# Kernel optimization log

Measured on AMD Instinct MI355X. Metric: run time of the kernel, lower is better.

The kernel has to match this reference:

```python
import jax, jax.numpy as jnp
import numpy as np

H, T, D = 16, 2048, 1024
DH = D // H  # 64


def setup_inputs() -> dict:
    key = jax.random.key(0)
    ks = jax.random.split(key, 6)
    state = jax.random.normal(ks[0], (H, DH, DH), jnp.float32) * 0.02  # per-head recurrent state
    x = jax.random.normal(ks[1], (T, D), jnp.float32)
    done = jax.random.uniform(ks[2], (T,)) < (4.0 / T)  # sparse episode-reset flags (bool)
    w_qkv = jax.random.normal(ks[3], (D, 3 * D), jnp.float32) / np.sqrt(D)
    b_qkv = jnp.zeros((3 * D,), jnp.float32)
    w_out = jax.random.normal(ks[4], (D, D), jnp.float32) / np.sqrt(D)
    b_out = jnp.zeros((D,), jnp.float32)
    return {"state": state, "x": x, "done": done, "w_qkv": w_qkv,
            "b_qkv": b_qkv, "w_out": w_out, "b_out": b_out}


def _mha_forward(state, x, done, w_qkv, b_qkv, w_out, b_out):
    # qkv projection; einops 'T (QKV H Dh) -> QKV H T Dh'
    qkv = (x @ w_qkv + b_qkv).reshape(T, 3, H, DH).transpose(1, 2, 0, 3)
    q, k, v = qkv[0], qkv[1], qkv[2]  # each (H, T, Dh)

    cum = jnp.cumsum(done.astype(jnp.int32))  # inclusive cumsum, as in done.cumsum()
    before_first = cum == 0            # tokens before first reset (attend to carried state)
    after_last = cum == cum[-1]        # tokens after last reset (feed new state)
    done_any = cum[-1] > 0

    # make_attn_mask(done): causal AND no reset index i with s < i <= t.
    # The scanned mask equals: causal & (cum[t] == cum[s]) (same-segment).
    t_idx = jnp.arange(T)
    mask = (t_idx[:, None] >= t_idx[None, :]) & (cum[:, None] == cum[None, :])  # (T, T)

    attn = jnp.where(mask[None], jnp.einsum('htd,hsd->hts', q, k), 0.0)  # mask * (q @ k.T)
    q_bef = q * before_first[None, :, None]
    out = jnp.einsum('hts,hsd->htd', attn, v) + jnp.einsum('htd,hde->hte', q_bef, state)

    k_aft = k * after_last[None, :, None]
    v_aft = v * after_last[None, :, None]
    s_new = jnp.einsum('htd,hte->hde', k_aft, v_aft)  # k_aft.T @ v_aft per head
    new_state = jnp.where(done_any, s_new, state + s_new)

    # 'H T Dh -> T (H Dh)' then output projection
    x_out = out.transpose(1, 0, 2).reshape(T, D) @ w_out + b_out
    return new_state, x_out


def reference(state, x, done, w_qkv, b_qkv, w_out, b_out):
    return _mha_forward(state, x, done, w_qkv, b_qkv, w_out, b_out)
```

## Files before the change

### kernel.cpp

```cpp
#include <hip/hip_runtime.h>

#define TT 2048
#define DD 1024
#define HH 16
#define DH 64
#define QKV_N 3072
#define QKW 2048

typedef __attribute__((ext_vector_type(8))) short bf16x8;
typedef __attribute__((ext_vector_type(4))) short short4v;
typedef __attribute__((ext_vector_type(4))) float f32x4;

__device__ inline short f2bf(float f) {
    union { float f; unsigned u; } v; v.f = f;
    unsigned r = v.u + 0x7fff + ((v.u >> 16) & 1);
    return (short)(r >> 16);
}

__device__ inline f32x4 mfma16(bf16x8 a, bf16x8 b, f32x4 c) {
    return __builtin_amdgcn_mfma_f32_16x16x32_bf16(a, b, c, 0, 0, 0);
}

__device__ __forceinline__ void gload16(const void* g, void* l) {
    __builtin_amdgcn_global_load_lds(
        (const __attribute__((address_space(1))) unsigned int*)g,
        (__attribute__((address_space(3))) unsigned int*)l, 16, 0, 0);
}

__device__ void transpose_tile(const float* __restrict__ in, short* __restrict__ out,
                               int R, int C, int r0, int c0, float (*tile)[65]) {
    int tid = threadIdx.x;
#pragma unroll
    for (int p = 0; p < 4; ++p) {
        int ch = tid + p * 256;
        int r = ch >> 4, c4 = (ch & 15) * 4;
        float4 v = *(const float4*)&in[(size_t)(r0 + r) * C + c0 + c4];
        tile[r][c4] = v.x; tile[r][c4 + 1] = v.y; tile[r][c4 + 2] = v.z; tile[r][c4 + 3] = v.w;
    }
    __syncthreads();
#pragma unroll
    for (int p = 0; p < 2; ++p) {
        int ch = tid + p * 256;
        int c = ch >> 3, r8 = (ch & 7) * 8;
        short tmp[8];
#pragma unroll
        for (int i = 0; i < 8; ++i) tmp[i] = f2bf(tile[r8 + i][c]);
        *(float4*)&out[(size_t)(c0 + c) * R + r0 + r8] = *(float4*)tmp;
    }
}

__global__ __launch_bounds__(256) void prep_kernel(const float* __restrict__ x,
                                                   const float* __restrict__ w_qkv,
                                                   const float* __restrict__ w_out,
                                                   const float* __restrict__ state,
                                                   const int* __restrict__ done,
                                                   short* __restrict__ x_bf,
                                                   short* __restrict__ wqT,
                                                   short* __restrict__ woT,
                                                   short* __restrict__ stT,
                                                   float* __restrict__ stout,
                                                   int* __restrict__ seg,
                                                   int* __restrict__ totalp,
                                                   int* __restrict__ aux) {
    __shared__ float tile[64][65];
    __shared__ int scanbuf[2048 + 512 + 1];
    int b = blockIdx.x;
    int tid = threadIdx.x;
    if (b < 1024) {
        int i = (b * 256 + tid) * 8;
        float4 a = *(const float4*)&x[i];
        float4 c = *(const float4*)&x[i + 4];
        short tmp[8] = {f2bf(a.x), f2bf(a.y), f2bf(a.z), f2bf(a.w),
                        f2bf(c.x), f2bf(c.y), f2bf(c.z), f2bf(c.w)};
        *(float4*)&x_bf[i] = *(float4*)tmp;
    } else if (b < 1792) {
        int bb = b - 1024;
        transpose_tile(w_qkv, wqT, DD, QKV_N, (bb & 15) * 64, (bb >> 4) * 64, tile);
    } else if (b < 2048) {
        int bb = b - 1792;
        transpose_tile(w_out, woT, DD, DD, (bb & 15) * 64, (bb >> 4) * 64, tile);
    } else if (b < 2064) {
        int h = b - 2048;
        transpose_tile(state + (size_t)h * 4096, stT + (size_t)h * 4096, DH, DH, 0, 0, tile);
    } else if (b < 2128) {
        __shared__ int anyf;
        if (tid == 0) anyf = 0;
        __syncthreads();
        int acc = 0;
#pragma unroll
        for (int i = 0; i < 8; ++i) acc |= done[tid * 8 + i];
        if (acc) anyf = 1;
        __syncthreads();
        int f = ((b - 2064) * 256 + tid) * 4;
        float4 v = anyf ? make_float4(0.f, 0.f, 0.f, 0.f) : *(const float4*)&state[f];
        *(float4*)&stout[f] = v;
    } else {
        int* segl = scanbuf;
        int* part = scanbuf + 2048;
        int* excl = scanbuf + 2304;
        int base = tid * 8;
        int local[8];
        int run = 0;
#pragma unroll
        for (int i = 0; i < 8; ++i) { run += (done[base + i] != 0) ? 1 : 0; local[i] = run; }
        part[tid] = run;
        __syncthreads();
        if (tid < 64) {
            int p4[4];
#pragma unroll
            for (int i = 0; i < 4; ++i) p4[i] = part[tid * 4 + i];
            int s = p4[0] + p4[1] + p4[2] + p4[3];
            int v = s;
#pragma unroll
            for (int off = 1; off < 64; off <<= 1) {
                int u = __shfl_up(v, off);
                if (tid >= off) v += u;
            }
            int ex = v - s;
#pragma unroll
            for (int i = 0; i < 4; ++i) { excl[tid * 4 + i] = ex; ex += p4[i]; }
            if (tid == 63) { totalp[0] = v; scanbuf[2560] = v; }
        }
        __syncthreads();
        int off = excl[tid];
#pragma unroll
        for (int i = 0; i < 8; ++i) {
            int sv = off + local[i];
            seg[base + i] = sv;
            segl[base + i] = sv;
        }
        __syncthreads();
        if (tid < 33) {
            int target = (tid < 32) ? segl[tid * 64] : scanbuf[2560];
            int lo = 0, hi = 2047;
            while (lo < hi) { int mid = (lo + hi) >> 1; if (segl[mid] >= target) hi = mid; else lo = mid + 1; }
            aux[tid] = lo >> 6;
        }
    }
}

__global__ __launch_bounds__(256) void gemm_qkv(const short* __restrict__ A,
                                                const short* __restrict__ BT,
                                                const float* __restrict__ bias,
                                                short* __restrict__ qk,
                                                short* __restrict__ vt) {
    __shared__ __align__(16) short As[128 * 32];
    __shared__ __align__(16) short Bs[128 * 32];
    const int K = DD;
    int tid = threadIdx.x;
    int wave = tid >> 6, lane = tid & 63;
    int quad = lane >> 4, l15 = lane & 15;
    int m0 = blockIdx.x * 128, n0 = blockIdx.y * 128;
    int wr = (wave >> 1) * 64, wc = (wave & 1) * 64;

    int srow = wave * 16 + (lane >> 2);
    int scol = (lane & 3) * 8;
    const short* Ag = A + (size_t)(m0 + srow) * K + scol;
    const short* Bg = BT + (size_t)(n0 + srow) * K + scol;
    short* As0 = &As[(wave * 16) * 32];
    short* As1 = &As[(64 + wave * 16) * 32];
    short* Bs0 = &Bs[(wave * 16) * 32];
    short* Bs1 = &Bs[(64 + wave * 16) * 32];

    f32x4 acc[4][4] = {};
    for (int k0 = 0; k0 < K; k0 += 32) {
        __syncthreads();
        gload16(Ag + k0, As0);
        gload16(Ag + (size_t)64 * K + k0, As1);
        gload16(Bg + k0, Bs0);
        gload16(Bg + (size_t)64 * K + k0, Bs1);
        __syncthreads();
        bf16x8 af[4], bfr[4];
#pragma unroll
        for (int i = 0; i < 4; ++i) {
            af[i]  = *(const bf16x8*)&As[(wr + i * 16 + l15) * 32 + quad * 8];
            bfr[i] = *(const bf16x8*)&Bs[(wc + i * 16 + l15) * 32 + quad * 8];
        }
#pragma unroll
        for (int i = 0; i < 4; ++i)
#pragma unroll
            for (int j = 0; j < 4; ++j)
                acc[i][j] = mfma16(af[i], bfr[j], acc[i][j]);
    }

    if (n0 < 2048) {
#pragma unroll
        for (int i = 0; i < 4; ++i)
#pragma unroll
            for (int j = 0; j < 4; ++j)
#pragma unroll
                for (int r = 0; r < 4; ++r) {
                    int row = m0 + wr + i * 16 + quad * 4 + r;
                    int col = n0 + wc + j * 16 + l15;
                    qk[(size_t)row * QKW + col] = f2bf(acc[i][j][r] + bias[col]);
                }
    } else {
#pragma unroll
        for (int j = 0; j < 4; ++j) {
            int col = n0 + wc + j * 16 + l15;
            float bv = bias[col];
            int eg = col - 2048;
            int hh = eg >> 6, e = eg & 63;
#pragma unroll
            for (int i = 0; i < 4; ++i) {
                int tb = m0 + wr + i * 16 + quad * 4;
                short4v pk;
#pragma unroll
                for (int r = 0; r < 4; ++r) pk[r] = f2bf(acc[i][j][r] + bv);
                *(short4v*)&vt[(size_t)hh * (DH * TT) + (size_t)e * TT + tb] = pk;
            }
        }
    }
}

__global__ __launch_bounds__(256) void attn_mfma(const short* __restrict__ qk,
                                                 const short* __restrict__ vt,
                                                 const short* __restrict__ stT,
                                                 const int* __restrict__ seg,
                                                 const int* __restrict__ totalp,
                                                 const int* __restrict__ aux,
                                                 short* __restrict__ outb,
                                                 float* __restrict__ nsout) {
    __shared__ __align__(16) short Qh[2][128 * 32];
    __shared__ __align__(16) short Kh[2][2][64 * 32];
    __shared__ __align__(16) short Vh[2][2][64 * 32];
    __shared__ __align__(16) short Ss[128 * 72];

    int h = blockIdx.x, tb = blockIdx.y;
    int t0 = tb * 128;
    int tid = threadIdx.x, wave = tid >> 6, lane = tid & 63;
    int quad = lane >> 4, l15 = lane & 15;
    int myt = wave * 32;
    const short* vbase = vt + (size_t)h * (DH * TT);

    if (blockIdx.z == 1) {
        int total = totalp[0];
        int myd = wave * 16;
        short* KhS0 = Kh[0][0];
        short* KhS1 = Kh[0][1];
#pragma unroll
        for (int cc = 0; cc < 2; ++cc) {
            int ct = tb * 2 + cc;
            if (ct < aux[32]) continue;
            int t0c = ct * 64;
            bool keep = (seg[t0c + lane] == total);
            const short* src = qk + (size_t)(t0c + lane) * QKW + 1024 + h * DH + myd;
            union { float4 f; short s[8]; } u0, u1;
            u0.f = keep ? *(const float4*)src : make_float4(0.f, 0.f, 0.f, 0.f);
            u1.f = keep ? *(const float4*)(src + 8) : make_float4(0.f, 0.f, 0.f, 0.f);
            short* dst = (lane < 32) ? &KhS0[lane] : &KhS1[lane - 32];
#pragma unroll
            for (int i = 0; i < 8; ++i) {
                dst[(myd + i) * 32] = u0.s[i];
                dst[(myd + 8 + i) * 32] = u1.s[i];
            }
            bf16x8 a0 = *(const bf16x8*)&KhS0[(myd + l15) * 32 + quad * 8];
            bf16x8 a1 = *(const bf16x8*)&KhS1[(myd + l15) * 32 + quad * 8];
            f32x4 acc2[4] = {};
#pragma unroll
            for (int j = 0; j < 4; ++j) {
                const short* vrow = vbase + (size_t)(j * 16 + l15) * TT + t0c + quad * 8;
                bf16x8 b0 = *(const bf16x8*)vrow;
                bf16x8 b1 = *(const bf16x8*)(vrow + 32);
                acc2[j] = mfma16(a0, b0, acc2[j]);
                acc2[j] = mfma16(a1, b1, acc2[j]);
            }
            float* oh = nsout + (size_t)h * 4096;
#pragma unroll
            for (int j = 0; j < 4; ++j)
#pragma unroll
                for (int r = 0; r < 4; ++r)
                    atomicAdd(&oh[(myd + quad * 4 + r) * DH + j * 16 + l15], acc2[j][r]);
        }
        return;
    }

    int st0 = aux[2 * tb];
    int st_hi = 2 * tb + 1;

    int srow = wave * 16 + (lane >> 2);
    int chunk = (lane & 3);
    const short* kg = qk + 1024 + h * DH;

    {
        int sr = (lane >> 2);
#pragma unroll
        for (int h2 = 0; h2 < 2; ++h2)
#pragma unroll
            for (int q = 0; q < 2; ++q)
                gload16(qk + (size_t)(t0 + myt + q * 16 + sr) * QKW + h * DH + h2 * 32 + chunk * 8,
                        &Qh[h2][(myt + q * 16) * 32]);
        int s0 = st0 * 64;
        gload16(kg + (size_t)(s0 + srow) * QKW + chunk * 8,      &Kh[0][0][(wave * 16) * 32]);
        gload16(kg + (size_t)(s0 + srow) * QKW + 32 + chunk * 8, &Kh[0][1][(wave * 16) * 32]);
        gload16(vbase + (size_t)srow * TT + s0 + chunk * 8,      &Vh[0][0][(wave * 16) * 32]);
        gload16(vbase + (size_t)srow * TT + s0 + 32 + chunk * 8, &Vh[0][1][(wave * 16) * 32]);
    }
    __syncthreads();

    bf16x8 af[2][2];
#pragma unroll
    for (int i = 0; i < 2; ++i)
#pragma unroll
        for (int h2 = 0; h2 < 2; ++h2)
            af[i][h2] = *(const bf16x8*)&Qh[h2][(myt + i * 16 + l15) * 32 + quad * 8];

    int seg_lane[2], t_val[2];
#pragma unroll
    for (int i = 0; i < 2; ++i) {
        t_val[i] = t0 + myt + i * 16 + l15;
        seg_lane[i] = seg[t_val[i]];
    }

    f32x4 acc2[4][2] = {};
    if (seg[t0] == 0) {
        const short* sb = stT + (size_t)h * 4096;
#pragma unroll
        for (int j = 0; j < 4; ++j)
#pragma unroll
            for (int h2 = 0; h2 < 2; ++h2) {
                bf16x8 a = *(const bf16x8*)(sb + (j * 16 + l15) * 64 + h2 * 32 + quad * 8);
#pragma unroll
                for (int i = 0; i < 2; ++i)
                    acc2[j][i] = mfma16(a, af[i][h2], acc2[j][i]);
            }
#pragma unroll
        for (int i = 0; i < 2; ++i)
            if (seg_lane[i] != 0)
#pragma unroll
                for (int j = 0; j < 4; ++j)
#pragma unroll
                    for (int r = 0; r < 4; ++r) acc2[j][i][r] = 0.f;
    }

    int p = 0;
    for (int st = st0; st <= st_hi; ++st, p ^= 1) {
        if (st != st0) __syncthreads();
        if (st + 1 <= st_hi) {
            int s1 = (st + 1) * 64;
            gload16(kg + (size_t)(s1 + srow) * QKW + chunk * 8,      &Kh[p ^ 1][0][(wave * 16) * 32]);
            gload16(kg + (size_t)(s1 + srow) * QKW + 32 + chunk * 8, &Kh[p ^ 1][1][(wave * 16) * 32]);
            gload16(vbase + (size_t)srow * TT + s1 + chunk * 8,      &Vh[p ^ 1][0][(wave * 16) * 32]);
            gload16(vbase + (size_t)srow * TT + s1 + 32 + chunk * 8, &Vh[p ^ 1][1][(wave * 16) * 32]);
        }
        int s0 = st * 64;

        f32x4 sacc[2][4] = {};
#pragma unroll
        for (int j = 0; j < 4; ++j)
#pragma unroll
            for (int h2 = 0; h2 < 2; ++h2) {
                bf16x8 kb = *(const bf16x8*)&Kh[p][h2][(j * 16 + l15) * 32 + quad * 8];
#pragma unroll
                for (int i = 0; i < 2; ++i)
                    sacc[i][j] = mfma16(kb, af[i][h2], sacc[i][j]);
            }
        int4 seg4[4];
#pragma unroll
        for (int j = 0; j < 4; ++j)
            seg4[j] = *(const int4*)&seg[s0 + j * 16 + quad * 4];
#pragma unroll
        for (int i = 0; i < 2; ++i)
#pragma unroll
            for (int j = 0; j < 4; ++j) {
                short4v pk;
#pragma unroll
                for (int r = 0; r < 4; ++r) {
                    int s_val = s0 + j * 16 + quad * 4 + r;
                    int sv = (r == 0) ? seg4[j].x : (r == 1) ? seg4[j].y : (r == 2) ? seg4[j].z : seg4[j].w;
                    bool ok = (sv == seg_lane[i]) && (s_val <= t_val[i]);
                    pk[r] = ok ? f2bf(sacc[i][j][r]) : (short)0;
                }
                *(short4v*)&Ss[(myt + i * 16 + l15) * 72 + j * 16 + quad * 4] = pk;
            }
        bf16x8 sf[2][2];
#pragma unroll
        for (int i = 0; i < 2; ++i)
#pragma unroll
            for (int h2 = 0; h2 < 2; ++h2)
                sf[i][h2] = *(const bf16x8*)&Ss[(myt + i * 16 + l15) * 72 + h2 * 32 + quad * 8];
#pragma unroll
        for (int j = 0; j < 4; ++j)
#pragma unroll
            for (int h2 = 0; h2 < 2; ++h2) {
                bf16x8 vb = *(const bf16x8*)&Vh[p][h2][(j * 16 + l15) * 32 + quad * 8];
#pragma unroll
                for (int i = 0; i < 2; ++i)
                    acc2[j][i] = mfma16(vb, sf[i][h2], acc2[j][i]);
            }
    }

#pragma unroll
    for (int i = 0; i < 2; ++i)
#pragma unroll
        for (int j = 0; j < 4; ++j) {
            short4v pk;
#pragma unroll
            for (int r = 0; r < 4; ++r) pk[r] = f2bf(acc2[j][i][r]);
            *(short4v*)&outb[(size_t)t_val[i] * DD + h * DH + j * 16 + quad * 4] = pk;
        }
}

__global__ __launch_bounds__(256) void gemm_out(const short* __restrict__ A,
                                                const short* __restrict__ BT,
                                                const float* __restrict__ bias,
                                                float* __restrict__ Cout,
                                                int M, int N, int K) {
    __shared__ __align__(16) short As[128 * 32];
    __shared__ __align__(16) short Bs[128 * 32];
    int tid = threadIdx.x;
    int wave = tid >> 6, lane = tid & 63;
    int quad = lane >> 4, l15 = lane & 15;
    int m0 = blockIdx.x * 128, n0 = blockIdx.y * 128;
    int wr = (wave >> 1) * 64, wc = (wave & 1) * 64;

    int srow = wave * 16 + (lane >> 2);
    int scol = (lane & 3) * 8;
    const short* Ag = A + (size_t)(m0 + srow) * K + scol;
    const short* Bg = BT + (size_t)(n0 + srow) * K + scol;
    short* As0 = &As[(wave * 16) * 32];
    short* As1 = &As[(64 + wave * 16) * 32];
    short* Bs0 = &Bs[(wave * 16) * 32];
    short* Bs1 = &Bs[(64 + wave * 16) * 32];

    f32x4 acc[4][4] = {};
    for (int k0 = 0; k0 < K; k0 += 32) {
        __syncthreads();
        gload16(Ag + k0, As0);
        gload16(Ag + (size_t)64 * K + k0, As1);
        gload16(Bg + k0, Bs0);
        gload16(Bg + (size_t)64 * K + k0, Bs1);
        __syncthreads();
        bf16x8 af[4], bfr[4];
#pragma unroll
        for (int i = 0; i < 4; ++i) {
            af[i]  = *(const bf16x8*)&As[(wr + i * 16 + l15) * 32 + quad * 8];
            bfr[i] = *(const bf16x8*)&Bs[(wc + i * 16 + l15) * 32 + quad * 8];
        }
#pragma unroll
        for (int i = 0; i < 4; ++i)
#pragma unroll
            for (int j = 0; j < 4; ++j)
                acc[i][j] = mfma16(af[i], bfr[j], acc[i][j]);
    }
#pragma unroll
    for (int i = 0; i < 4; ++i)
#pragma unroll
        for (int j = 0; j < 4; ++j)
#pragma unroll
            for (int r = 0; r < 4; ++r) {
                int row = m0 + wr + i * 16 + quad * 4 + r;
                int col = n0 + wc + j * 16 + l15;
                Cout[(size_t)row * N + col] = acc[i][j][r] + bias[col];
            }
}

extern "C" void kernel_launch(void* const* d_in, const int* in_sizes, int n_in,
                              void* d_out, int out_size, void* d_ws, size_t ws_size,
                              hipStream_t stream) {
    const float* state = (const float*)d_in[0];
    const float* x     = (const float*)d_in[1];
    const int*   done  = (const int*)d_in[2];
    const float* w_qkv = (const float*)d_in[3];
    const float* b_qkv = (const float*)d_in[4];
    const float* w_out = (const float*)d_in[5];
    const float* b_out = (const float*)d_in[6];

    char* ws = (char*)d_ws;
    int*   seg    = (int*)ws;
    int*   totalp = (int*)(ws + 8192);
    int*   aux    = (int*)(ws + 8256);
    short* wqT    = (short*)(ws + 8448);
    short* woT    = (short*)(ws + 6299904);
    short* stT    = (short*)(ws + 8397056);
    short* qk     = (short*)(ws + 8528128);
    short* vt     = (short*)(ws + 16916736);
    short* xbf_outb = (short*)(ws + 21111040);

    float* new_state_out = (float*)d_out;
    float* x_out         = (float*)d_out + HH * DH * DH;

    prep_kernel<<<2129, 256, 0, stream>>>(x, w_qkv, w_out, state, done,
                                          xbf_outb, wqT, woT, stT,
                                          new_state_out, seg, totalp, aux);

    gemm_qkv<<<dim3(TT / 128, QKV_N / 128), 256, 0, stream>>>(
        xbf_outb, wqT, b_qkv, qk, vt);

    attn_mfma<<<dim3(HH, TT / 128, 2), 256, 0, stream>>>(
        qk, vt, stT, seg, totalp, aux, xbf_outb, new_state_out);

    gemm_out<<<dim3(TT / 128, DD / 128), 256, 0, stream>>>(
        xbf_outb, woT, b_out, x_out, TT, DD, DD);
}
```

Baseline: 163.5 us.

## Split attention over key chunks with partial reduce, split-K output GEMM, wider QKV K-step

Attention now uses 64-token query tiles and splits the key range of each tile into chunks along grid z, writing fp32 partials that a new reduce kernel sums. The state-update path moves to its own z slice. The output GEMM becomes split-K by two with atomicAdd into an output that prep_kernel pre-fills with the bias. The QKV GEMM loads 64-wide K tiles per sync to halve barrier count. The aim is more parallelism and fewer idle CUs, at the cost of extra partial-buffer traffic, atomics and one more launch.

Result: faster. 159.4 us (-2.5%).

```diff
diff --git a/kernel.cpp b/kernel.cpp
--- a/kernel.cpp
+++ b/kernel.cpp
@@ -54,11 +54,13 @@
                                                    const float* __restrict__ w_out,
                                                    const float* __restrict__ state,
                                                    const int* __restrict__ done,
+                                                   const float* __restrict__ b_out,
                                                    short* __restrict__ x_bf,
                                                    short* __restrict__ wqT,
                                                    short* __restrict__ woT,
                                                    short* __restrict__ stT,
                                                    float* __restrict__ stout,
+                                                   float* __restrict__ x_out,
                                                    int* __restrict__ seg,
                                                    int* __restrict__ totalp,
                                                    int* __restrict__ aux) {
@@ -94,6 +96,10 @@
         int f = ((b - 2064) * 256 + tid) * 4;
         float4 v = anyf ? make_float4(0.f, 0.f, 0.f, 0.f) : *(const float4*)&state[f];
         *(float4*)&stout[f] = v;
+    } else if (b < 4176) {
+        int f = ((b - 2128) * 256 + tid) * 4;
+        int col = f & (DD - 1);
+        *(float4*)&x_out[f] = *(const float4*)&b_out[col];
     } else {
         int* segl = scanbuf;
         int* part = scanbuf + 2048;
@@ -144,13 +150,285 @@
                                                 const float* __restrict__ bias,
                                                 short* __restrict__ qk,
                                                 short* __restrict__ vt) {
-    __shared__ __align__(16) short As[128 * 32];
-    __shared__ __align__(16) short Bs[128 * 32];
+    __shared__ __align__(16) short As[2][128 * 32];
+    __shared__ __align__(16) short Bs[2][128 * 32];
     const int K = DD;
     int tid = threadIdx.x;
     int wave = tid >> 6, lane = tid & 63;
     int quad = lane >> 4, l15 = lane & 15;
     int m0 = blockIdx.x * 128, n0 = blockIdx.y * 128;
+    int wr = (wave >> 1) * 64, wc = (wave & 1) * 64;
+
+    int srow = wave * 32 + (lane >> 2);
+    int scol = (lane & 3) * 8;
+    const short* Ag = A + (size_t)(m0 + srow) * K + scol;
+    const short* Bg = BT + (size_t)(n0 + srow) * K + scol;
+
+    f32x4 acc[4][4] = {};
+    for (int k0 = 0; k0 < K; k0 += 64) {
+        __syncthreads();
+#pragma unroll
+        for (int g = 0; g < 2; ++g)
+#pragma unroll
+            for (int ks = 0; ks < 2; ++ks) {
+                gload16(Ag + (size_t)g * 16 * K + k0 + ks * 32, &As[ks][(wave * 32 + g * 16) * 32]);
+                gload16(Bg + (size_t)g * 16 * K + k0 + ks * 32, &Bs[ks][(wave * 32 + g * 16) * 32]);
+            }
+        __syncthreads();
+#pragma unroll
+        for (int ks = 0; ks < 2; ++ks) {
+            bf16x8 af[4], bfr[4];
+#pragma unroll
+            for (int i = 0; i < 4; ++i) {
+                af[i]  = *(const bf16x8*)&As[ks][(wr + i * 16 + l15) * 32 + quad * 8];
+                bfr[i] = *(const bf16x8*)&Bs[ks][(wc + i * 16 + l15) * 32 + quad * 8];
+            }
+#pragma unroll
+            for (int i = 0; i < 4; ++i)
+#pragma unroll
+                for (int j = 0; j < 4; ++j)
+                    acc[i][j] = mfma16(af[i], bfr[j], acc[i][j]);
+        }
+    }
+
+    if (n0 < 2048) {
+#pragma unroll
+        for (int i = 0; i < 4; ++i)
+#pragma unroll
+            for (int j = 0; j < 4; ++j)
+#pragma unroll
+                for (int r = 0; r < 4; ++r) {
+                    int row = m0 + wr + i * 16 + quad * 4 + r;
+                    int col = n0 + wc + j * 16 + l15;
+                    qk[(size_t)row * QKW + col] = f2bf(acc[i][j][r] + bias[col]);
+                }
+    } else {
+#pragma unroll
+        for (int j = 0; j < 4; ++j) {
+            int col = n0 + wc + j * 16 + l15;
+            float bv = bias[col];
+            int eg = col - 2048;
+            int hh = eg >> 6, e = eg & 63;
+#pragma unroll
+            for (int i = 0; i < 4; ++i) {
+                int tb = m0 + wr + i * 16 + quad * 4;
+                short4v pk;
+#pragma unroll
+                for (int r = 0; r < 4; ++r) pk[r] = f2bf(acc[i][j][r] + bv);
+                *(short4v*)&vt[(size_t)hh * (DH * TT) + (size_t)e * TT + tb] = pk;
+            }
+        }
+    }
+}
+
+__global__ __launch_bounds__(256) void attn_mfma(const short* __restrict__ qk,
+                                                 const short* __restrict__ vt,
+                                                 const short* __restrict__ stT,
+                                                 const int* __restrict__ seg,
+                                                 const int* __restrict__ totalp,
+                                                 const int* __restrict__ aux,
+                                                 short* __restrict__ outb,
+                                                 float* __restrict__ part,
+                                                 float* __restrict__ nsout) {
+    __shared__ __align__(16) short Qh[2][64 * 32];
+    __shared__ __align__(16) short Kh[2][2][64 * 32];
+    __shared__ __align__(16) short Vh[2][2][64 * 32];
+    __shared__ __align__(16) short Ss[64 * 72];
+
+    int h = blockIdx.x, tt = blockIdx.y, z = blockIdx.z;
+    int t0 = tt * 64;
+    int tid = threadIdx.x, wave = tid >> 6, lane = tid & 63;
+    int quad = lane >> 4, l15 = lane & 15;
+    int myt = wave * 16;
+    const short* vbase = vt + (size_t)h * (DH * TT);
+
+    if (z == 8) {
+        if (tt < aux[32]) return;
+        int total = totalp[0];
+        int myd = wave * 16;
+        short* K0 = Kh[0][0];
+        short* K1 = Kh[0][1];
+        bool keep = (seg[t0 + lane] == total);
+        const short* src = qk + (size_t)(t0 + lane) * QKW + 1024 + h * DH + myd;
+        union { float4 f; short s[8]; } u0, u1;
+        u0.f = keep ? *(const float4*)src : make_float4(0.f, 0.f, 0.f, 0.f);
+        u1.f = keep ? *(const float4*)(src + 8) : make_float4(0.f, 0.f, 0.f, 0.f);
+        short* dst = (lane < 32) ? &K0[lane] : &K1[lane - 32];
+#pragma unroll
+        for (int i = 0; i < 8; ++i) {
+            dst[(myd + i) * 32] = u0.s[i];
+            dst[(myd + 8 + i) * 32] = u1.s[i];
+        }
+        bf16x8 a0 = *(const bf16x8*)&K0[(myd + l15) * 32 + quad * 8];
+        bf16x8 a1 = *(const bf16x8*)&K1[(myd + l15) * 32 + quad * 8];
+        f32x4 acc2[4] = {};
+#pragma unroll
+        for (int j = 0; j < 4; ++j) {
+            const short* vrow = vbase + (size_t)(j * 16 + l15) * TT + t0 + quad * 8;
+            bf16x8 b0 = *(const bf16x8*)vrow;
+            bf16x8 b1 = *(const bf16x8*)(vrow + 32);
+            acc2[j] = mfma16(a0, b0, acc2[j]);
+            acc2[j] = mfma16(a1, b1, acc2[j]);
+        }
+        float* oh = nsout + (size_t)h * 4096;
+#pragma unroll
+        for (int j = 0; j < 4; ++j)
+#pragma unroll
+            for (int r = 0; r < 4; ++r)
+                atomicAdd(&oh[(myd + quad * 4 + r) * DH + j * 16 + l15], acc2[j][r]);
+        return;
+    }
+
+    int st0 = aux[tt];
+    int sc_lo = st0 >> 2, sc_hi = tt >> 2;
+    if (z < sc_lo || z > sc_hi) return;
+    bool direct = (sc_lo == sc_hi);
+    int st_lo = (st0 > z * 4) ? st0 : z * 4;
+    int st_hi = (tt < z * 4 + 3) ? tt : z * 4 + 3;
+
+    int sr = lane >> 2;
+    int ch = lane & 3;
+    const short* kg = qk + 1024 + h * DH;
+
+    {
+#pragma unroll
+        for (int h2 = 0; h2 < 2; ++h2)
+            gload16(qk + (size_t)(t0 + myt + sr) * QKW + h * DH + h2 * 32 + ch * 8,
+                    &Qh[h2][myt * 32]);
+        int s0 = st_lo * 64;
+        gload16(kg + (size_t)(s0 + myt + sr) * QKW + ch * 8,      &Kh[0][0][myt * 32]);
+        gload16(kg + (size_t)(s0 + myt + sr) * QKW + 32 + ch * 8, &Kh[0][1][myt * 32]);
+        gload16(vbase + (size_t)(myt + sr) * TT + s0 + ch * 8,    &Vh[0][0][myt * 32]);
+        gload16(vbase + (size_t)(myt + sr) * TT + s0 + 32 + ch * 8, &Vh[0][1][myt * 32]);
+    }
+    __syncthreads();
+
+    bf16x8 af[2];
+#pragma unroll
+    for (int h2 = 0; h2 < 2; ++h2)
+        af[h2] = *(const bf16x8*)&Qh[h2][(myt + l15) * 32 + quad * 8];
+
+    int t_val = t0 + myt + l15;
+    int seg_lane = seg[t_val];
+
+    f32x4 acc2[4] = {};
+    if (z == sc_lo && seg[t0] == 0) {
+        const short* sb = stT + (size_t)h * 4096;
+#pragma unroll
+        for (int j = 0; j < 4; ++j)
+#pragma unroll
+            for (int h2 = 0; h2 < 2; ++h2) {
+                bf16x8 a = *(const bf16x8*)(sb + (j * 16 + l15) * 64 + h2 * 32 + quad * 8);
+                acc2[j] = mfma16(a, af[h2], acc2[j]);
+            }
+        if (seg_lane != 0) {
+#pragma unroll
+            for (int j = 0; j < 4; ++j)
+#pragma unroll
+                for (int r = 0; r < 4; ++r) acc2[j][r] = 0.f;
+        }
+    }
+
+    int p = 0;
+    for (int st = st_lo; st <= st_hi; ++st, p ^= 1) {
+        if (st != st_lo) __syncthreads();
+        if (st + 1 <= st_hi) {
+            int s1 = (st + 1) * 64;
+            gload16(kg + (size_t)(s1 + myt + sr) * QKW + ch * 8,        &Kh[p ^ 1][0][myt * 32]);
+            gload16(kg + (size_t)(s1 + myt + sr) * QKW + 32 + ch * 8,   &Kh[p ^ 1][1][myt * 32]);
+            gload16(vbase + (size_t)(myt + sr) * TT + s1 + ch * 8,      &Vh[p ^ 1][0][myt * 32]);
+            gload16(vbase + (size_t)(myt + sr) * TT + s1 + 32 + ch * 8, &Vh[p ^ 1][1][myt * 32]);
+        }
+        int s0 = st * 64;
+
+        f32x4 sacc[4] = {};
+#pragma unroll
+        for (int j = 0; j < 4; ++j)
+#pragma unroll
+            for (int h2 = 0; h2 < 2; ++h2) {
+                bf16x8 kb = *(const bf16x8*)&Kh[p][h2][(j * 16 + l15) * 32 + quad * 8];
+                sacc[j] = mfma16(kb, af[h2], sacc[j]);
+            }
+        int4 seg4[4];
+#pragma unroll
+        for (int j = 0; j < 4; ++j)
+            seg4[j] = *(const int4*)&seg[s0 + j * 16 + quad * 4];
+#pragma unroll
+        for (int j = 0; j < 4; ++j) {
+            short4v pk;
+#pragma unroll
+            for (int r = 0; r < 4; ++r) {
+                int s_val = s0 + j * 16 + quad * 4 + r;
+                int sv = (r == 0) ? seg4[j].x : (r == 1) ? seg4[j].y : (r == 2) ? seg4[j].z : seg4[j].w;
+                bool ok = (sv == seg_lane) && (s_val <= t_val);
+                pk[r] = ok ? f2bf(sacc[j][r]) : (short)0;
+            }
+            *(short4v*)&Ss[(myt + l15) * 72 + j * 16 + quad * 4] = pk;
+        }
+        bf16x8 sf[2];
+#pragma unroll
+        for (int h2 = 0; h2 < 2; ++h2)
+            sf[h2] = *(const bf16x8*)&Ss[(myt + l15) * 72 + h2 * 32 + quad * 8];
+#pragma unroll
+        for (int j = 0; j < 4; ++j)
+#pragma unroll
+            for (int h2 = 0; h2 < 2; ++h2) {
+                bf16x8 vb = *(const bf16x8*)&Vh[p][h2][(j * 16 + l15) * 32 + quad * 8];
+                acc2[j] = mfma16(vb, sf[h2], acc2[j]);
+            }
+    }
+
+    if (direct) {
+#pragma unroll
+        for (int j = 0; j < 4; ++j) {
+            short4v pk;
+#pragma unroll
+            for (int r = 0; r < 4; ++r) pk[r] = f2bf(acc2[j][r]);
+            *(short4v*)&outb[(size_t)t_val * DD + h * DH + j * 16 + quad * 4] = pk;
+        }
+    } else {
+        float* pb = part + ((size_t)((h * 32 + tt) * 8 + z)) * 4096;
+#pragma unroll
+        for (int j = 0; j < 4; ++j)
+            *(f32x4*)&pb[(myt + l15) * 64 + j * 16 + quad * 4] = acc2[j];
+    }
+}
+
+__global__ __launch_bounds__(256) void attn_reduce(const float* __restrict__ part,
+                                                   const int* __restrict__ aux,
+                                                   short* __restrict__ outb) {
+    int h = blockIdx.x, tt = blockIdx.y;
+    int sc_lo = aux[tt] >> 2, sc_hi = tt >> 2;
+    if (sc_lo == sc_hi) return;
+    int t0 = tt * 64;
+    int tid = threadIdx.x;
+    const float* pb = part + ((size_t)(h * 32 + tt) * 8) * 4096;
+#pragma unroll
+    for (int p = 0; p < 4; ++p) {
+        int idx = p * 256 + tid;
+        int row = idx >> 4, c4 = (idx & 15) * 4;
+        float4 acc = make_float4(0.f, 0.f, 0.f, 0.f);
+        for (int sc = sc_lo; sc <= sc_hi; ++sc) {
+            float4 v = *(const float4*)&pb[(size_t)sc * 4096 + row * 64 + c4];
+            acc.x += v.x; acc.y += v.y; acc.z += v.z; acc.w += v.w;
+        }
+        short4v pk;
+        pk[0] = f2bf(acc.x); pk[1] = f2bf(acc.y); pk[2] = f2bf(acc.z); pk[3] = f2bf(acc.w);
+        *(short4v*)&outb[(size_t)(t0 + row) * DD + h * DH + c4] = pk;
+    }
+}
+
+__global__ __launch_bounds__(256) void gemm_out(const short* __restrict__ A,
+                                                const short* __restrict__ BT,
+                                                float* __restrict__ Cout,
+                                                int M, int N, int K) {
+    __shared__ __align__(16) short As[128 * 32];
+    __shared__ __align__(16) short Bs[128 * 32];
+    int tid = threadIdx.x;
+    int wave = tid >> 6, lane = tid & 63;
+    int quad = lane >> 4, l15 = lane & 15;
+    int m0 = blockIdx.x * 128, n0 = blockIdx.y * 128;
+    int kb0 = blockIdx.z * (K / 2), kb1 = kb0 + K / 2;
     int wr = (wave >> 1) * 64, wc = (wave & 1) * 64;
 
     int srow = wave * 16 + (lane >> 2);
@@ -163,7 +441,7 @@
     short* Bs1 = &Bs[(64 + wave * 16) * 32];
 
     f32x4 acc[4][4] = {};
-    for (int k0 = 0; k0 < K; k0 += 32) {
+    for (int k0 = kb0; k0 < kb1; k0 += 32) {
         __syncthreads();
         gload16(Ag + k0, As0);
         gload16(Ag + (size_t)64 * K + k0, As1);
@@ -182,267 +460,6 @@
             for (int j = 0; j < 4; ++j)
                 acc[i][j] = mfma16(af[i], bfr[j], acc[i][j]);
     }
-
-    if (n0 < 2048) {
-#pragma unroll
-        for (int i = 0; i < 4; ++i)
-#pragma unroll
-            for (int j = 0; j < 4; ++j)
-#pragma unroll
-                for (int r = 0; r < 4; ++r) {
-                    int row = m0 + wr + i * 16 + quad * 4 + r;
-                    int col = n0 + wc + j * 16 + l15;
-                    qk[(size_t)row * QKW + col] = f2bf(acc[i][j][r] + bias[col]);
-                }
-    } else {
-#pragma unroll
-        for (int j = 0; j < 4; ++j) {
-            int col = n0 + wc + j * 16 + l15;
-            float bv = bias[col];
-            int eg = col - 2048;
-            int hh = eg >> 6, e = eg & 63;
-#pragma unroll
-            for (int i = 0; i < 4; ++i) {
-                int tb = m0 + wr + i * 16 + quad * 4;
-                short4v pk;
-#pragma unroll
-                for (int r = 0; r < 4; ++r) pk[r] = f2bf(acc[i][j][r] + bv);
-                *(short4v*)&vt[(size_t)hh * (DH * TT) + (size_t)e * TT + tb] = pk;
-            }
-        }
-    }
-}
-
-__global__ __launch_bounds__(256) void attn_mfma(const short* __restrict__ qk,
-                                                 const short* __restrict__ vt,
-                                                 const short* __restrict__ stT,
-                                                 const int* __restrict__ seg,
-                                                 const int* __restrict__ totalp,
-                                                 const int* __restrict__ aux,
-                                                 short* __restrict__ outb,
-                                                 float* __restrict__ nsout) {
-    __shared__ __align__(16) short Qh[2][128 * 32];
-    __shared__ __align__(16) short Kh[2][2][64 * 32];
-    __shared__ __align__(16) short Vh[2][2][64 * 32];
-    __shared__ __align__(16) short Ss[128 * 72];
-
-    int h = blockIdx.x, tb = blockIdx.y;
-    int t0 = tb * 128;
-    int tid = threadIdx.x, wave = tid >> 6, lane = tid & 63;
-    int quad = lane >> 4, l15 = lane & 15;
-    int myt = wave * 32;
-    const short* vbase = vt + (size_t)h * (DH * TT);
-
-    if (blockIdx.z == 1) {
-        int total = totalp[0];
-        int myd = wave * 16;
-        short* KhS0 = Kh[0][0];
-        short* KhS1 = Kh[0][1];
-#pragma unroll
-        for (int cc = 0; cc < 2; ++cc) {
-            int ct = tb * 2 + cc;
-            if (ct < aux[32]) continue;
-            int t0c = ct * 64;
-            bool keep = (seg[t0c + lane] == total);
-            const short* src = qk + (size_t)(t0c + lane) * QKW + 1024 + h * DH + myd;
-            union { float4 f; short s[8]; } u0, u1;
-            u0.f = keep ? *(const float4*)src : make_float4(0.f, 0.f, 0.f, 0.f);
-            u1.f = keep ? *(const float4*)(src + 8) : make_float4(0.f, 0.f, 0.f, 0.f);
-            short* dst = (lane < 32) ? &KhS0[lane] : &KhS1[lane - 32];
-#pragma unroll
-            for (int i = 0; i < 8; ++i) {
-                dst[(myd + i) * 32] = u0.s[i];
-                dst[(myd + 8 + i) * 32] = u1.s[i];
-            }
-            bf16x8 a0 = *(const bf16x8*)&KhS0[(myd + l15) * 32 + quad * 8];
-            bf16x8 a1 = *(const bf16x8*)&KhS1[(myd + l15) * 32 + quad * 8];
-            f32x4 acc2[4] = {};
-#pragma unroll
-            for (int j = 0; j < 4; ++j) {
-                const short* vrow = vbase + (size_t)(j * 16 + l15) * TT + t0c + quad * 8;
-                bf16x8 b0 = *(const bf16x8*)vrow;
-                bf16x8 b1 = *(const bf16x8*)(vrow + 32);
-                acc2[j] = mfma16(a0, b0, acc2[j]);
-                acc2[j] = mfma16(a1, b1, acc2[j]);
-            }
-            float* oh = nsout + (size_t)h * 4096;
-#pragma unroll
-            for (int j = 0; j < 4; ++j)
-#pragma unroll
-                for (int r = 0; r < 4; ++r)
-                    atomicAdd(&oh[(myd + quad * 4 + r) * DH + j * 16 + l15], acc2[j][r]);
-        }
-        return;
-    }
-
-    int st0 = aux[2 * tb];
-    int st_hi = 2 * tb + 1;
-
-    int srow = wave * 16 + (lane >> 2);
-    int chunk = (lane & 3);
-    const short* kg = qk + 1024 + h * DH;
-
-    {
-        int sr = (lane >> 2);
-#pragma unroll
-        for (int h2 = 0; h2 < 2; ++h2)
-#pragma unroll
-            for (int q = 0; q < 2; ++q)
-                gload16(qk + (size_t)(t0 + myt + q * 16 + sr) * QKW + h * DH + h2 * 32 + chunk * 8,
-                        &Qh[h2][(myt + q * 16) * 32]);
-        int s0 = st0 * 64;
-        gload16(kg + (size_t)(s0 + srow) * QKW + chunk * 8,      &Kh[0][0][(wave * 16) * 32]);
-        gload16(kg + (size_t)(s0 + srow) * QKW + 32 + chunk * 8, &Kh[0][1][(wave * 16) * 32]);
-        gload16(vbase + (size_t)srow * TT + s0 + chunk * 8,      &Vh[0][0][(wave * 16) * 32]);
-        gload16(vbase + (size_t)srow * TT + s0 + 32 + chunk * 8, &Vh[0][1][(wave * 16) * 32]);
-    }
-    __syncthreads();
-
-    bf16x8 af[2][2];
-#pragma unroll
-    for (int i = 0; i < 2; ++i)
-#pragma unroll
-        for (int h2 = 0; h2 < 2; ++h2)
-            af[i][h2] = *(const bf16x8*)&Qh[h2][(myt + i * 16 + l15) * 32 + quad * 8];
-
-    int seg_lane[2], t_val[2];
-#pragma unroll
-    for (int i = 0; i < 2; ++i) {
-        t_val[i] = t0 + myt + i * 16 + l15;
-        seg_lane[i] = seg[t_val[i]];
-    }
-
-    f32x4 acc2[4][2] = {};
-    if (seg[t0] == 0) {
-        const short* sb = stT + (size_t)h * 4096;
-#pragma unroll
-        for (int j = 0; j < 4; ++j)
-#pragma unroll
-            for (int h2 = 0; h2 < 2; ++h2) {
-                bf16x8 a = *(const bf16x8*)(sb + (j * 16 + l15) * 64 + h2 * 32 + quad * 8);
-#pragma unroll
-                for (int i = 0; i < 2; ++i)
-                    acc2[j][i] = mfma16(a, af[i][h2], acc2[j][i]);
-            }
-#pragma unroll
-        for (int i = 0; i < 2; ++i)
-            if (seg_lane[i] != 0)
-#pragma unroll
-                for (int j = 0; j < 4; ++j)
-#pragma unroll
-                    for (int r = 0; r < 4; ++r) acc2[j][i][r] = 0.f;
-    }
-
-    int p = 0;
-    for (int st = st0; st <= st_hi; ++st, p ^= 1) {
-        if (st != st0) __syncthreads();
-        if (st + 1 <= st_hi) {
-            int s1 = (st + 1) * 64;
-            gload16(kg + (size_t)(s1 + srow) * QKW + chunk * 8,      &Kh[p ^ 1][0][(wave * 16) * 32]);
-            gload16(kg + (size_t)(s1 + srow) * QKW + 32 + chunk * 8, &Kh[p ^ 1][1][(wave * 16) * 32]);
-            gload16(vbase + (size_t)srow * TT + s1 + chunk * 8,      &Vh[p ^ 1][0][(wave * 16) * 32]);
-            gload16(vbase + (size_t)srow * TT + s1 + 32 + chunk * 8, &Vh[p ^ 1][1][(wave * 16) * 32]);
-        }
-        int s0 = st * 64;
-
-        f32x4 sacc[2][4] = {};
-#pragma unroll
-        for (int j = 0; j < 4; ++j)
-#pragma unroll
-            for (int h2 = 0; h2 < 2; ++h2) {
-                bf16x8 kb = *(const bf16x8*)&Kh[p][h2][(j * 16 + l15) * 32 + quad * 8];
-#pragma unroll
-                for (int i = 0; i < 2; ++i)
-                    sacc[i][j] = mfma16(kb, af[i][h2], sacc[i][j]);
-            }
-        int4 seg4[4];
-#pragma unroll
-        for (int j = 0; j < 4; ++j)
-            seg4[j] = *(const int4*)&seg[s0 + j * 16 + quad * 4];
-#pragma unroll
-        for (int i = 0; i < 2; ++i)
-#pragma unroll
-            for (int j = 0; j < 4; ++j) {
-                short4v pk;
-#pragma unroll
-                for (int r = 0; r < 4; ++r) {
-                    int s_val = s0 + j * 16 + quad * 4 + r;
-                    int sv = (r == 0) ? seg4[j].x : (r == 1) ? seg4[j].y : (r == 2) ? seg4[j].z : seg4[j].w;
-                    bool ok = (sv == seg_lane[i]) && (s_val <= t_val[i]);
-                    pk[r] = ok ? f2bf(sacc[i][j][r]) : (short)0;
-                }
-                *(short4v*)&Ss[(myt + i * 16 + l15) * 72 + j * 16 + quad * 4] = pk;
-            }
-        bf16x8 sf[2][2];
-#pragma unroll
-        for (int i = 0; i < 2; ++i)
-#pragma unroll
-            for (int h2 = 0; h2 < 2; ++h2)
-                sf[i][h2] = *(const bf16x8*)&Ss[(myt + i * 16 + l15) * 72 + h2 * 32 + quad * 8];
-#pragma unroll
-        for (int j = 0; j < 4; ++j)
-#pragma unroll
-            for (int h2 = 0; h2 < 2; ++h2) {
-                bf16x8 vb = *(const bf16x8*)&Vh[p][h2][(j * 16 + l15) * 32 + quad * 8];
-#pragma unroll
-                for (int i = 0; i < 2; ++i)
-                    acc2[j][i] = mfma16(vb, sf[i][h2], acc2[j][i]);
-            }
-    }
-
-#pragma unroll
-    for (int i = 0; i < 2; ++i)
-#pragma unroll
-        for (int j = 0; j < 4; ++j) {
-            short4v pk;
-#pragma unroll
-            for (int r = 0; r < 4; ++r) pk[r] = f2bf(acc2[j][i][r]);
-            *(short4v*)&outb[(size_t)t_val[i] * DD + h * DH + j * 16 + quad * 4] = pk;
-        }
-}
-
-__global__ __launch_bounds__(256) void gemm_out(const short* __restrict__ A,
-                                                const short* __restrict__ BT,
-                                                const float* __restrict__ bias,
-                                                float* __restrict__ Cout,
-                                                int M, int N, int K) {
-    __shared__ __align__(16) short As[128 * 32];
-    __shared__ __align__(16) short Bs[128 * 32];
-    int tid = threadIdx.x;
-    int wave = tid >> 6, lane = tid & 63;
-    int quad = lane >> 4, l15 = lane & 15;
-    int m0 = blockIdx.x * 128, n0 = blockIdx.y * 128;
-    int wr = (wave >> 1) * 64, wc = (wave & 1) * 64;
-
-    int srow = wave * 16 + (lane >> 2);
-    int scol = (lane & 3) * 8;
-    const short* Ag = A + (size_t)(m0 + srow) * K + scol;
-    const short* Bg = BT + (size_t)(n0 + srow) * K + scol;
-    short* As0 = &As[(wave * 16) * 32];
-    short* As1 = &As[(64 + wave * 16) * 32];
-    short* Bs0 = &Bs[(wave * 16) * 32];
-    short* Bs1 = &Bs[(64 + wave * 16) * 32];
-
-    f32x4 acc[4][4] = {};
-    for (int k0 = 0; k0 < K; k0 += 32) {
-        __syncthreads();
-        gload16(Ag + k0, As0);
-        gload16(Ag + (size_t)64 * K + k0, As1);
-        gload16(Bg + k0, Bs0);
-        gload16(Bg + (size_t)64 * K + k0, Bs1);
-        __syncthreads();
-        bf16x8 af[4], bfr[4];
-#pragma unroll
-        for (int i = 0; i < 4; ++i) {
-            af[i]  = *(const bf16x8*)&As[(wr + i * 16 + l15) * 32 + quad * 8];
-            bfr[i] = *(const bf16x8*)&Bs[(wc + i * 16 + l15) * 32 + quad * 8];
-        }
-#pragma unroll
-        for (int i = 0; i < 4; ++i)
-#pragma unroll
-            for (int j = 0; j < 4; ++j)
-                acc[i][j] = mfma16(af[i], bfr[j], acc[i][j]);
-    }
 #pragma unroll
     for (int i = 0; i < 4; ++i)
 #pragma unroll
@@ -451,7 +468,7 @@
             for (int r = 0; r < 4; ++r) {
                 int row = m0 + wr + i * 16 + quad * 4 + r;
                 int col = n0 + wc + j * 16 + l15;
-                Cout[(size_t)row * N + col] = acc[i][j][r] + bias[col];
+                atomicAdd(&Cout[(size_t)row * N + col], acc[i][j][r]);
             }
 }
 
@@ -476,20 +493,23 @@
     short* qk     = (short*)(ws + 8528128);
     short* vt     = (short*)(ws + 16916736);
     short* xbf_outb = (short*)(ws + 21111040);
+    float* part   = (float*)(ws + 25305344);
 
     float* new_state_out = (float*)d_out;
     float* x_out         = (float*)d_out + HH * DH * DH;
 
-    prep_kernel<<<2129, 256, 0, stream>>>(x, w_qkv, w_out, state, done,
+    prep_kernel<<<4177, 256, 0, stream>>>(x, w_qkv, w_out, state, done, b_out,
                                           xbf_outb, wqT, woT, stT,
-                                          new_state_out, seg, totalp, aux);
+                                          new_state_out, x_out, seg, totalp, aux);
 
     gemm_qkv<<<dim3(TT / 128, QKV_N / 128), 256, 0, stream>>>(
         xbf_outb, wqT, b_qkv, qk, vt);
 
-    attn_mfma<<<dim3(HH, TT / 128, 2), 256, 0, stream>>>(
-        qk, vt, stT, seg, totalp, aux, xbf_outb, new_state_out);
-
-    gemm_out<<<dim3(TT / 128, DD / 128), 256, 0, stream>>>(
-        xbf_outb, woT, b_out, x_out, TT, DD, DD);
-}
+    attn_mfma<<<dim3(HH, TT / 64, 9), 256, 0, stream>>>(
+        qk, vt, stT, seg, totalp, aux, xbf_outb, part, new_state_out);
+
+    attn_reduce<<<dim3(HH, TT / 64), 256, 0, stream>>>(part, aux, xbf_outb);
+
+    gemm_out<<<dim3(TT / 128, DD / 128, 2), 256, 0, stream>>>(
+        xbf_outb, woT, x_out, TT, DD, DD);
+}
```
